# Performance work log

Measured on AMD Instinct MI355X. Metric: run time of the kernel, lower is better.

## Reference

```python
import jax, jax.numpy as jnp
import numpy as np

RES = 300          # grid resolution per axis
NC_D = 16          # density_n_comp
NC_A = 48          # app_n_comp
APP_DIM = 27       # app_dim
N = 500000         # number of ray samples

MAT_MODE = [[0, 1], [0, 2], [1, 2]]
VEC_MODE = [2, 1, 0]


def setup_inputs() -> dict:
    key = jax.random.key(0)
    k0, k1, k2, k3 = jax.random.split(key, 4)
    xyz_sampled = jax.random.uniform(k0, (N, 3), minval=-1.0, maxval=1.0, dtype=jnp.float32)
    plane_coef = 0.1 * jax.random.normal(k1, (3, NC_A + NC_D, RES, RES), dtype=jnp.float32)
    line_coef = 0.1 * jax.random.normal(k2, (3, NC_A + NC_D, RES, 1), dtype=jnp.float32)
    basis_W = jax.random.normal(k3, (APP_DIM, 3 * NC_A), dtype=jnp.float32) / np.sqrt(3 * NC_A)
    return {"xyz_sampled": xyz_sampled, "plane_coef": plane_coef,
            "line_coef": line_coef, "basis_W": basis_W}


def _grid_sample(img, x, y):
    """Bilinear grid_sample, align_corners=True, zeros padding.
    img: (C, H, W); x, y: (N,) normalized coords in [-1, 1] (x -> W, y -> H).
    Returns (C, N)."""
    C, H, W = img.shape
    ix = (x + 1.0) * 0.5 * (W - 1)
    iy = (y + 1.0) * 0.5 * (H - 1)
    x0f = jnp.floor(ix)
    y0f = jnp.floor(iy)
    wx = ix - x0f   # weight for x0+1
    wy = iy - y0f   # weight for y0+1
    x0 = x0f.astype(jnp.int32)
    y0 = y0f.astype(jnp.int32)
    out = jnp.zeros((C, x.shape[0]), img.dtype)
    for dx, wxc in ((0, 1.0 - wx), (1, wx)):
        for dy, wyc in ((0, 1.0 - wy), (1, wy)):
            xi = x0 + dx
            yi = y0 + dy
            valid = (xi >= 0) & (xi < W) & (yi >= 0) & (yi < H)
            xic = jnp.clip(xi, 0, W - 1)
            yic = jnp.clip(yi, 0, H - 1)
            w = jnp.where(valid, wxc * wyc, 0.0)
            out = out + img[:, yic, xic] * w
    return out


def reference(xyz_sampled, plane_coef, line_coef, basis_W):
    zeros = jnp.zeros((xyz_sampled.shape[0],), xyz_sampled.dtype)
    pf, lf = [], []
    for i in range(3):
        m0, m1 = MAT_MODE[i]
        # plane: grid = (x=xyz[m0] -> W, y=xyz[m1] -> H)
        pf.append(_grid_sample(plane_coef[i], xyz_sampled[:, m0], xyz_sampled[:, m1]))
        # line: grid = (x=0 -> W(=1), y=xyz[vecMode] -> H) => 1D interp along H
        lf.append(_grid_sample(line_coef[i], zeros, xyz_sampled[:, VEC_MODE[i]]))
    pf = jnp.stack(pf)  # (3, NC_A+NC_D, N)
    lf = jnp.stack(lf)  # (3, NC_A+NC_D, N)
    # compute_densityfeature: last density_n_comp channels, multiply and sum-reduce
    sigma_feature = jnp.sum(pf[:, NC_A:] * lf[:, NC_A:], axis=(0, 1))  # (N,)
    # compute_appfeature: first app_n_comp channels, multiply then basis projection
    app_feats = (pf[:, :NC_A] * lf[:, :NC_A]).reshape(3 * NC_A, -1)    # (3*NC_A, N)
    app_features = app_feats.T @ basis_W.T                              # (N, APP_DIM)
    return sigma_feature, app_features
```

## Files before the change

### kernel.cpp

```cpp
#include <hip/hip_runtime.h>
#include <hip/hip_bf16.h>

#define RES 300
#define NPLANE (RES * RES)
#define NC_A 48
#define APP_DIM 27
#define KDIM 144
#define KS 168

#define PT_TILES 1407
#define NPB2 (3 * PT_TILES)

__device__ __forceinline__ float bf_lo(unsigned int u) { return __uint_as_float(u << 16); }
__device__ __forceinline__ float bf_hi(unsigned int u) { return __uint_as_float(u & 0xffff0000u); }

__global__ __launch_bounds__(256) void prep(
    const float* __restrict__ plane, const float* __restrict__ line,
    const float* __restrict__ W,
    unsigned int* __restrict__ TpUo, unsigned int* __restrict__ TlP,
    __hip_bfloat16* __restrict__ Wg) {
  __shared__ __align__(16) unsigned int lt[64 * 65];
  const int blk = blockIdx.x;
  const int tid = threadIdx.x;

  if (blk < NPB2) {
    const int i  = blk / PT_TILES;
    const int t0 = blk - i * PT_TILES;
    const int p0 = t0 * 64;

    const int cb   = (tid >> 4) * 4;
    const int poff = (tid & 15) * 4;
    const bool ok  = (p0 + poff) < NPLANE;

    const float* src = plane + (size_t)(i * 64 + cb) * NPLANE + p0 + poff;
    float4 v0, v1, v2, v3;
    v0 = v1 = v2 = v3 = make_float4(0.f, 0.f, 0.f, 0.f);
    if (ok) {
      v0 = *(const float4*)(src);
      v1 = *(const float4*)(src + NPLANE);
      v2 = *(const float4*)(src + 2 * NPLANE);
      v3 = *(const float4*)(src + 3 * NPLANE);
    }
    const int col = (tid >> 4) * 2;
    const float* f0 = &v0.x; const float* f1 = &v1.x;
    const float* f2 = &v2.x; const float* f3 = &v3.x;
    #pragma unroll
    for (int j = 0; j < 4; ++j) {
      __hip_bfloat162 ha, hb;
      ha.x = __float2bfloat16(f0[j]);
      ha.y = __float2bfloat16(f1[j]);
      hb.x = __float2bfloat16(f2[j]);
      hb.y = __float2bfloat16(f3[j]);
      uint2 u;
      u.x = *(unsigned int*)&ha;
      u.y = *(unsigned int*)&hb;
      *(uint2*)&lt[(poff + j) * 34 + col] = u;
    }
    __syncthreads();
    #pragma unroll
    for (int pass = 0; pass < 2; ++pass) {
      int p  = (tid >> 3) + pass * 32;
      int c4 = (tid & 7) * 4;
      if (p0 + p < NPLANE) {
        uint2 a = *(const uint2*)&lt[p * 34 + c4];
        uint2 b = *(const uint2*)&lt[p * 34 + c4 + 2];
        uint4 w; w.x = a.x; w.y = a.y; w.z = b.x; w.w = b.y;
        *(uint4*)&TpUo[((size_t)(i * NPLANE + p0 + p)) * 32 + c4] = w;
      }
    }
  } else if (blk < NPB2 + 15) {
    const int b  = blk - NPB2;
    const int i  = b / 5;
    const int y0 = (b % 5) * 64;
    const int yl = tid & 63;
    const int cq = tid >> 6;
    #pragma unroll
    for (int k = 0; k < 16; ++k) {
      int c = cq * 16 + k;
      int y = y0 + yl;
      float a = 0.f, bv = 0.f;
      if (y < RES) {
        const float* row = line + (i * 64 + c) * RES;
        a  = row[y];
        bv = row[min(y + 1, RES - 1)];
      }
      __hip_bfloat162 h;
      h.x = __float2bfloat16(a);
      h.y = __float2bfloat16(bv);
      lt[yl * 65 + c] = *(unsigned int*)&h;
    }
    __syncthreads();
    #pragma unroll
    for (int k = 0; k < 16; ++k) {
      int ylc = k * 4 + cq;
      int c   = tid & 63;
      int y   = y0 + ylc;
      if (y < RES) TlP[((size_t)i * RES + y) * 64 + c] = lt[ylc * 65 + c];
    }
  } else {
    for (int idx = tid; idx < 2 * 5 * 64 * 8; idx += 256) {
      int j    = idx & 7;
      int lane = (idx >> 3) & 63;
      int kt   = (idx >> 9) % 5;
      int tile = idx / (5 * 64 * 8);
      int n = tile * 16 + (lane & 15);
      int k = kt * 32 + (lane >> 4) * 8 + j;
      float v = (n < APP_DIM && k < KDIM) ? W[n * KDIM + k] : 0.f;
      Wg[idx] = __float2bfloat16(v);
    }
  }
}

typedef __attribute__((ext_vector_type(8))) short short8;
typedef __attribute__((ext_vector_type(4))) float f32x4;

__global__ __launch_bounds__(256, 5) void tensorf_main(
    const float* __restrict__ xyz, const unsigned int* __restrict__ TpU,
    const unsigned int* __restrict__ TlP, const __hip_bfloat16* __restrict__ Wg,
    float* __restrict__ out, int n_total) {
  __shared__ __hip_bfloat16 prod[64 * KS];
  __shared__ float cw[64 * 18];

  const int tid  = threadIdx.x;
  const int lane = tid & 63;
  const int wave = tid >> 6;
  const int n0   = blockIdx.x * 64;

  for (int j = tid; j < 64 * 12; j += 256) {
    int s = j / 12, kk = (j % 12) * 2;
    *(unsigned int*)&prod[s * KS + KDIM + kk] = 0u;
  }

  if (tid < 64) {
    int n = min(n0 + tid, n_total - 1);
    float crd[3] = {xyz[3 * n], xyz[3 * n + 1], xyz[3 * n + 2]};
    const int m0s[3] = {0, 0, 1}, m1s[3] = {1, 2, 2}, vms[3] = {2, 1, 0};
    float* c = &cw[tid * 18];
    #pragma unroll
    for (int i = 0; i < 3; ++i) {
      float ix = fminf(fmaxf((crd[m0s[i]] + 1.f) * 149.5f, 0.f), 299.f);
      float iy = fminf(fmaxf((crd[m1s[i]] + 1.f) * 149.5f, 0.f), 299.f);
      float ly = fminf(fmaxf((crd[vms[i]] + 1.f) * 149.5f, 0.f), 299.f);
      float x0f = fminf(floorf(ix), 298.f);
      float y0f = fminf(floorf(iy), 298.f);
      float l0f = fminf(floorf(ly), 298.f);
      float wx = ix - x0f, wy = iy - y0f, lwy = ly - l0f;
      int cell = i * NPLANE + (int)y0f * RES + (int)x0f;
      int lidx = i * RES + (int)l0f;
      c[i * 6 + 0] = __int_as_float(cell | (lidx << 19));
      c[i * 6 + 1] = (1.f - wx) * (1.f - wy);
      c[i * 6 + 2] = wx * (1.f - wy);
      c[i * 6 + 3] = (1.f - wx) * wy;
      c[i * 6 + 4] = wx * wy;
      c[i * 6 + 5] = lwy;
    }
  }
  __syncthreads();

  const int cq = lane & 15;
  const int sq = lane >> 4;
  const int c4 = cq * 4;

  #pragma unroll 2
  for (int it = 0; it < 4; ++it) {
    const int s = wave * 16 + it * 4 + sq;
    const float* cp = &cw[s * 18];

    uint2 u00[3], u01[3], u10[3], u11[3];
    uint4 ul[3];
    float wgt[3][5];
    #pragma unroll
    for (int i = 0; i < 3; ++i) {
      float2 q0 = *(const float2*)&cp[i * 6];
      float2 q1 = *(const float2*)&cp[i * 6 + 2];
      float2 q2 = *(const float2*)&cp[i * 6 + 4];
      int pk   = __float_as_int(q0.x);
      int cell = pk & 0x7FFFF;
      int lidx = pk >> 19;
      int bidx = cell * 32 + cq * 2;
      u00[i] = *(const uint2*)&TpU[bidx];
      u01[i] = *(const uint2*)&TpU[bidx + 32];
      u10[i] = *(const uint2*)&TpU[bidx + RES * 32];
      u11[i] = *(const uint2*)&TpU[bidx + RES * 32 + 32];
      ul[i]  = *(const uint4*)&TlP[(lidx << 6) + c4];
      wgt[i][0] = q0.y; wgt[i][1] = q1.x; wgt[i][2] = q1.y;
      wgt[i][3] = q2.x; wgt[i][4] = q2.y;
    }

    float dsum = 0.f;
    #pragma unroll
    for (int i = 0; i < 3; ++i) {
      float w00 = wgt[i][0], w01 = wgt[i][1], w10 = wgt[i][2];
      float w11 = wgt[i][3], lw = wgt[i][4];
      {
        float pf_l = w00 * bf_lo(u00[i].x) + w01 * bf_lo(u01[i].x) +
                     w10 * bf_lo(u10[i].x) + w11 * bf_lo(u11[i].x);
        float pf_h = w00 * bf_hi(u00[i].x) + w01 * bf_hi(u01[i].x) +
                     w10 * bf_hi(u10[i].x) + w11 * bf_hi(u11[i].x);
        float lal = bf_lo(ul[i].x), lbl = bf_hi(ul[i].x);
        float lah = bf_lo(ul[i].y), lbh = bf_hi(ul[i].y);
        float lf_l = lal + lw * (lbl - lal);
        float lf_h = lah + lw * (lbh - lah);
        float prl = pf_l * lf_l, prh = pf_h * lf_h;
        if (cq < 12) {
          __hip_bfloat162 h;
          h.x = __float2bfloat16(prl);
          h.y = __float2bfloat16(prh);
          *(unsigned int*)&prod[s * KS + i * NC_A + c4] = *(unsigned int*)&h;
        } else {
          dsum += prl + prh;
        }
      }
      {
        float pf_l = w00 * bf_lo(u00[i].y) + w01 * bf_lo(u01[i].y) +
                     w10 * bf_lo(u10[i].y) + w11 * bf_lo(u11[i].y);
        float pf_h = w00 * bf_hi(u00[i].y) + w01 * bf_hi(u01[i].y) +
                     w10 * bf_hi(u10[i].y) + w11 * bf_hi(u11[i].y);
        float lal = bf_lo(ul[i].z), lbl = bf_hi(ul[i].z);
        float lah = bf_lo(ul[i].w), lbh = bf_hi(ul[i].w);
        float lf_l = lal + lw * (lbl - lal);
        float lf_h = lah + lw * (lbh - lah);
        float prl = pf_l * lf_l, prh = pf_h * lf_h;
        if (cq < 12) {
          __hip_bfloat162 h;
          h.x = __float2bfloat16(prl);
          h.y = __float2bfloat16(prh);
          *(unsigned int*)&prod[s * KS + i * NC_A + c4 + 2] = *(unsigned int*)&h;
        } else {
          dsum += prl + prh;
        }
      }
    }
    dsum += __shfl_xor(dsum, 1);
    dsum += __shfl_xor(dsum, 2);
    int n = n0 + s;
    if (cq == 12 && n < n_total) out[n] = dsum;
  }
  __syncthreads();

  const int srow = lane & 15, quad = lane >> 4;
  f32x4 acc0 = {0.f, 0.f, 0.f, 0.f}, acc1 = {0.f, 0.f, 0.f, 0.f};
  const short* prodS = (const short*)prod;
  const short* WgS   = (const short*)Wg;
  const int arow = (wave * 16 + srow) * KS;
  #pragma unroll
  for (int kt = 0; kt < 5; ++kt) {
    short8 a  = *(const short8*)&prodS[arow + kt * 32 + quad * 8];
    short8 b0 = *(const short8*)&WgS[(kt * 64 + lane) * 8];
    short8 b1 = *(const short8*)&WgS[((5 + kt) * 64 + lane) * 8];
    acc0 = __builtin_amdgcn_mfma_f32_16x16x32_bf16(a, b0, acc0, 0, 0, 0);
    acc1 = __builtin_amdgcn_mfma_f32_16x16x32_bf16(a, b1, acc1, 0, 0, 0);
  }
  float* outApp = out + n_total;
  #pragma unroll
  for (int r = 0; r < 4; ++r) {
    int n = n0 + wave * 16 + quad * 4 + r;
    if (n < n_total) {
      outApp[(size_t)n * APP_DIM + srow] = acc0[r];
      if (srow < APP_DIM - 16)
        outApp[(size_t)n * APP_DIM + 16 + srow] = acc1[r];
    }
  }
}

extern "C" void kernel_launch(void* const* d_in, const int* in_sizes, int n_in,
                              void* d_out, int out_size, void* d_ws, size_t ws_size,
                              hipStream_t stream) {
  const float* xyz   = (const float*)d_in[0];
  const float* plane = (const float*)d_in[1];
  const float* line  = (const float*)d_in[2];
  const float* W     = (const float*)d_in[3];
  float* out = (float*)d_out;
  const int N = in_sizes[0] / 3;

  char* ws = (char*)d_ws;
  __hip_bfloat16* Tp  = (__hip_bfloat16*)ws;
  unsigned int*   TlP = (unsigned int*)(ws + 34560000);
  __hip_bfloat16* Wg  = (__hip_bfloat16*)(ws + 34560000 + 230400);

  prep<<<NPB2 + 16, 256, 0, stream>>>(plane, line, W, (unsigned int*)Tp, TlP, Wg);
  tensorf_main<<<(N + 63) / 64, 256, 0, stream>>>(
      xyz, (const unsigned int*)Tp, TlP, Wg, out, N);
}
```

Measured before the change: 225.0 us.

## Sort samples by Morton-order spatial bins before gather and remap chunks per XCD

Adds a counting sort of the sample points into a 32^3 Morton-ordered bin grid (histogram, single-block scan, atomic scatter). The main kernel then processes samples in that sorted order and writes results back to each sample's original index. Blocks are also remapped so every XCD handles a contiguous range of sorted chunks, which should improve L2 locality for the plane gathers. The cost is four extra small launches, atomics, and scattered output writes.

```diff
diff --git a/kernel.cpp b/kernel.cpp
--- a/kernel.cpp
+++ b/kernel.cpp
@@ -7,12 +7,27 @@
 #define APP_DIM 27
 #define KDIM 144
 #define KS 168
+#define CWS 20
 
 #define PT_TILES 1407
 #define NPB2 (3 * PT_TILES)
 
+#define NBINS 32768
+
 __device__ __forceinline__ float bf_lo(unsigned int u) { return __uint_as_float(u << 16); }
 __device__ __forceinline__ float bf_hi(unsigned int u) { return __uint_as_float(u & 0xffff0000u); }
+
+__device__ __forceinline__ unsigned int spread5(unsigned int v) {
+  return (v & 1u) | ((v & 2u) << 2) | ((v & 4u) << 4) |
+         ((v & 8u) << 6) | ((v & 16u) << 8);
+}
+__device__ __forceinline__ unsigned int bin_key(float x, float y, float z) {
+  int qx = min(31, max(0, (int)((x + 1.f) * 16.f)));
+  int qy = min(31, max(0, (int)((y + 1.f) * 16.f)));
+  int qz = min(31, max(0, (int)((z + 1.f) * 16.f)));
+  return (spread5((unsigned)qz) << 2) | (spread5((unsigned)qy) << 1) |
+         spread5((unsigned)qx);
+}
 
 __global__ __launch_bounds__(256) void prep(
     const float* __restrict__ plane, const float* __restrict__ line,
@@ -111,20 +126,72 @@
   }
 }
 
+__global__ __launch_bounds__(256) void zero_hist(unsigned int* __restrict__ hist) {
+  hist[blockIdx.x * 256 + threadIdx.x] = 0u;
+}
+
+__global__ __launch_bounds__(256) void bin_hist(
+    const float* __restrict__ xyz, unsigned int* __restrict__ hist, int n_total) {
+  int n = blockIdx.x * 256 + threadIdx.x;
+  if (n < n_total) {
+    unsigned int k = bin_key(xyz[3 * n], xyz[3 * n + 1], xyz[3 * n + 2]);
+    atomicAdd(&hist[k], 1u);
+  }
+}
+
+__global__ __launch_bounds__(256) void bin_scan(unsigned int* __restrict__ hist) {
+  __shared__ unsigned int sums[256];
+  const int t = threadIdx.x;
+  unsigned int s = 0;
+  for (int k = 0; k < 128; ++k) s += hist[t * 128 + k];
+  sums[t] = s;
+  __syncthreads();
+  for (int off = 1; off < 256; off <<= 1) {
+    unsigned int v = (t >= off) ? sums[t - off] : 0u;
+    __syncthreads();
+    if (t >= off) sums[t] += v;
+    __syncthreads();
+  }
+  unsigned int excl = (t == 0) ? 0u : sums[t - 1];
+  for (int k = 0; k < 128; ++k) {
+    unsigned int h = hist[t * 128 + k];
+    hist[t * 128 + k] = excl;
+    excl += h;
+  }
+}
+
+__global__ __launch_bounds__(256) void bin_scatter(
+    const float* __restrict__ xyz, unsigned int* __restrict__ hist,
+    float4* __restrict__ xyzS, int n_total) {
+  int n = blockIdx.x * 256 + threadIdx.x;
+  if (n < n_total) {
+    float x = xyz[3 * n], y = xyz[3 * n + 1], z = xyz[3 * n + 2];
+    unsigned int k = bin_key(x, y, z);
+    unsigned int pos = atomicAdd(&hist[k], 1u);
+    float4 v; v.x = x; v.y = y; v.z = z; v.w = __int_as_float(n);
+    xyzS[pos] = v;
+  }
+}
+
 typedef __attribute__((ext_vector_type(8))) short short8;
 typedef __attribute__((ext_vector_type(4))) float f32x4;
 
 __global__ __launch_bounds__(256, 5) void tensorf_main(
-    const float* __restrict__ xyz, const unsigned int* __restrict__ TpU,
+    const float4* __restrict__ xyzS, const unsigned int* __restrict__ TpU,
     const unsigned int* __restrict__ TlP, const __hip_bfloat16* __restrict__ Wg,
     float* __restrict__ out, int n_total) {
   __shared__ __hip_bfloat16 prod[64 * KS];
-  __shared__ float cw[64 * 18];
+  __shared__ float cw[64 * CWS];
 
   const int tid  = threadIdx.x;
   const int lane = tid & 63;
   const int wave = tid >> 6;
-  const int n0   = blockIdx.x * 64;
+
+  const int nwg = gridDim.x;
+  const int qc  = nwg >> 3, rc = nwg & 7;
+  const int xcd = blockIdx.x & 7, kb = blockIdx.x >> 3;
+  const int chunk = (xcd < rc ? xcd * (qc + 1) : rc * (qc + 1) + (xcd - rc) * qc) + kb;
+  const int n0 = chunk * 64;
 
   for (int j = tid; j < 64 * 12; j += 256) {
     int s = j / 12, kk = (j % 12) * 2;
@@ -132,10 +199,10 @@
   }
 
   if (tid < 64) {
-    int n = min(n0 + tid, n_total - 1);
-    float crd[3] = {xyz[3 * n], xyz[3 * n + 1], xyz[3 * n + 2]};
+    float4 xs = xyzS[min(n0 + tid, n_total - 1)];
+    float crd[3] = {xs.x, xs.y, xs.z};
     const int m0s[3] = {0, 0, 1}, m1s[3] = {1, 2, 2}, vms[3] = {2, 1, 0};
-    float* c = &cw[tid * 18];
+    float* c = &cw[tid * CWS];
     #pragma unroll
     for (int i = 0; i < 3; ++i) {
       float ix = fminf(fmaxf((crd[m0s[i]] + 1.f) * 149.5f, 0.f), 299.f);
@@ -154,6 +221,7 @@
       c[i * 6 + 4] = wx * wy;
       c[i * 6 + 5] = lwy;
     }
+    c[18] = xs.w;
   }
   __syncthreads();
 
@@ -164,7 +232,7 @@
   #pragma unroll 2
   for (int it = 0; it < 4; ++it) {
     const int s = wave * 16 + it * 4 + sq;
-    const float* cp = &cw[s * 18];
+    const float* cp = &cw[s * CWS];
 
     uint2 u00[3], u01[3], u10[3], u11[3];
     uint4 ul[3];
@@ -233,8 +301,10 @@
     }
     dsum += __shfl_xor(dsum, 1);
     dsum += __shfl_xor(dsum, 2);
-    int n = n0 + s;
-    if (cq == 12 && n < n_total) out[n] = dsum;
+    if (cq == 12 && n0 + s < n_total) {
+      int pn = __float_as_int(cp[18]);
+      out[pn] = dsum;
+    }
   }
   __syncthreads();
 
@@ -254,11 +324,12 @@
   float* outApp = out + n_total;
   #pragma unroll
   for (int r = 0; r < 4; ++r) {
-    int n = n0 + wave * 16 + quad * 4 + r;
-    if (n < n_total) {
-      outApp[(size_t)n * APP_DIM + srow] = acc0[r];
+    int slot = wave * 16 + quad * 4 + r;
+    if (n0 + slot < n_total) {
+      int pn = __float_as_int(cw[slot * CWS + 18]);
+      outApp[(size_t)pn * APP_DIM + srow] = acc0[r];
       if (srow < APP_DIM - 16)
-        outApp[(size_t)n * APP_DIM + 16 + srow] = acc1[r];
+        outApp[(size_t)pn * APP_DIM + 16 + srow] = acc1[r];
     }
   }
 }
@@ -274,11 +345,17 @@
   const int N = in_sizes[0] / 3;
 
   char* ws = (char*)d_ws;
-  __hip_bfloat16* Tp  = (__hip_bfloat16*)ws;
-  unsigned int*   TlP = (unsigned int*)(ws + 34560000);
-  __hip_bfloat16* Wg  = (__hip_bfloat16*)(ws + 34560000 + 230400);
+  __hip_bfloat16* Tp   = (__hip_bfloat16*)ws;
+  unsigned int*   TlP  = (unsigned int*)(ws + 34560000);
+  __hip_bfloat16* Wg   = (__hip_bfloat16*)(ws + 34560000 + 230400);
+  unsigned int*   hist = (unsigned int*)(ws + 34800640);
+  float4*         xyzS = (float4*)(ws + 34931712);
 
   prep<<<NPB2 + 16, 256, 0, stream>>>(plane, line, W, (unsigned int*)Tp, TlP, Wg);
+  zero_hist<<<NBINS / 256, 256, 0, stream>>>(hist);
+  bin_hist<<<(N + 255) / 256, 256, 0, stream>>>(xyz, hist, N);
+  bin_scan<<<1, 256, 0, stream>>>(hist);
+  bin_scatter<<<(N + 255) / 256, 256, 0, stream>>>(xyz, hist, xyzS, N);
   tensorf_main<<<(N + 63) / 64, 256, 0, stream>>>(
-      xyz, (const unsigned int*)Tp, TlP, Wg, out, N);
-}
+      xyzS, (const unsigned int*)Tp, TlP, Wg, out, N);
+}
```

Measured after the change: 280.3 us. 24.6% more time.
